# Performance work log

Hardware: AMD Instinct MI355X
Metric: run time of the kernel (lower is better)

Reference implementation:

```python
import jax, jax.numpy as jnp
import numpy as np

N = 100000   # num nodes
E = 500000   # num hyperedges
NNZ = 1600000
H, C = 4, 32
IN_CH = 128


def setup_inputs() -> dict:
    key = jax.random.key(0)
    k1, k2, k3, k4, k5 = jax.random.split(key, 5)
    X = jax.random.normal(k1, (N, IN_CH), dtype=jnp.float32)
    W = jax.random.normal(k2, (IN_CH, H * C), dtype=jnp.float32) * (1.0 / np.sqrt(IN_CH))
    att_e = jax.random.normal(k3, (1, H, C), dtype=jnp.float32) * 0.1
    vertex = jax.random.randint(k4, (NNZ,), 0, N, dtype=jnp.int64)
    edges = jax.random.randint(k5, (NNZ,), 0, E, dtype=jnp.int64)
    return {"X": X, "W": W, "att_e": att_e, "vertex": vertex, "edges": edges}


def reference(X, W, att_e, vertex, edges):
    n = X.shape[0]
    X0 = X @ W                                  # [N, H*C]
    Xh = X0.reshape(n, H, C)                    # [N, H, C]
    Xve = Xh[vertex]                            # [nnz, H, C] gather
    # scatter-mean over hyperedges
    esum = jax.ops.segment_sum(Xve, edges, num_segments=E)            # [E, H, C]
    cnt = jax.ops.segment_sum(jnp.ones((Xve.shape[0],), X.dtype), edges, num_segments=E)
    Xe = esum / jnp.maximum(cnt, 1.0)[:, None, None]                  # [E, H, C]
    # per-edge attention score
    alpha_e = (Xe * att_e).sum(-1)              # [E, H]
    a_ev = alpha_e[edges]                       # [nnz, H]
    alpha = jax.nn.leaky_relu(a_ev, 0.01)
    # segment softmax over vertex groups
    m = jax.ops.segment_max(alpha, vertex, num_segments=n)            # [N, H]
    ex = jnp.exp(alpha - m[vertex])
    den = jax.ops.segment_sum(ex, vertex, num_segments=n)             # [N, H]
    alpha = ex / (den[vertex] + 1e-16)          # [nnz, H]
    # weighted scatter-sum back to nodes
    Xev = Xe[edges] * alpha[:, :, None]         # [nnz, H, C]
    Xv = jax.ops.segment_sum(Xev, vertex, num_segments=n)             # [N, H, C]
    return Xv.reshape(n, H * C) + X0
```

## Files before the change

kernel.cpp:

```cpp
#include <hip/hip_runtime.h>
#include <hip/hip_bf16.h>
#include <hip/hip_fp16.h>
#include <cstdint>

#define NH 4
#define HC 128
#define INCH 128
#define NEDGE 500000
#define NN 100000

#define KE_SHIFT 11
#define KV_SHIFT 9
#define KE (1 << KE_SHIFT)
#define KV (1 << KV_SHIFT)
#define NBE 245
#define NBV 196
#define CAP_E 8192
#define CAP_V 10240
#define CHUNK_A 8192

typedef float          f32x2 __attribute__((ext_vector_type(2)));
typedef float          f32x4 __attribute__((ext_vector_type(4)));
typedef float          f32x8 __attribute__((ext_vector_type(8)));
typedef unsigned int   u32x2 __attribute__((ext_vector_type(2)));
typedef unsigned int   u32x4 __attribute__((ext_vector_type(4)));
typedef unsigned short u16x8 __attribute__((ext_vector_type(8)));

static __device__ __forceinline__ unsigned short f2bf(float f){
  union { float f; unsigned u; } v; v.f = f;
  unsigned r = v.u + 0x7fffu + ((v.u >> 16) & 1u);
  return (unsigned short)(r >> 16);
}
static __device__ __forceinline__ float bf2f(unsigned short b){
  union { unsigned u; float f; } v; v.u = ((unsigned)b) << 16;
  return v.f;
}
static __device__ __forceinline__ f32x8 bf8f(u16x8 b){
  f32x8 r;
  r[0]=bf2f(b[0]); r[1]=bf2f(b[1]); r[2]=bf2f(b[2]); r[3]=bf2f(b[3]);
  r[4]=bf2f(b[4]); r[5]=bf2f(b[5]); r[6]=bf2f(b[6]); r[7]=bf2f(b[7]);
  return r;
}

#if __has_builtin(__builtin_amdgcn_cvt_pk_fp8_f32) && __has_builtin(__builtin_amdgcn_cvt_pk_f32_fp8)
#define FP8_HW 1
#else
#define FP8_HW 0
#endif

#if !FP8_HW
static __device__ __forceinline__ unsigned enc1_fp8(float v){
  union{ __half h; unsigned short u; } c; c.h = __float2half(v);
  unsigned u = c.u;
  unsigned s = (u>>15)&1u, e=(u>>10)&31u, m=u&0x3FFu;
  int e8 = (int)e - 8;
  unsigned lsb = (m>>7)&1u;
  unsigned m8 = (m + 63u + lsb) >> 7;
  if (m8 == 8u){ m8 = 0u; e8 += 1; }
  if (e8 <= 0)  return s<<7;
  if (e8 >= 16) return (s<<7)|0x7Eu;
  return (s<<7)|((unsigned)e8<<3)|m8;
}
static __device__ __forceinline__ float dec1_fp8(unsigned b){
  unsigned s=(b>>7)&1u, e=(b>>3)&15u, m=b&7u;
  union{unsigned u; float f;} r;
  if (e==0u){ r.f = (float)m * 0.001953125f; if(s) r.f = -r.f; }
  else r.u = (s<<31)|((e+120u)<<23)|(m<<20);
  return r.f;
}
#endif

static __device__ __forceinline__ u32x2 pack8_fp8(const f32x8 v){
  u32x2 w;
#if FP8_HW
  int w0 = __builtin_amdgcn_cvt_pk_fp8_f32(v[0], v[1], 0, false);
  w0     = __builtin_amdgcn_cvt_pk_fp8_f32(v[2], v[3], w0, true);
  int w1 = __builtin_amdgcn_cvt_pk_fp8_f32(v[4], v[5], 0, false);
  w1     = __builtin_amdgcn_cvt_pk_fp8_f32(v[6], v[7], w1, true);
  w.x = (unsigned)w0; w.y = (unsigned)w1;
#else
  w.x = enc1_fp8(v[0]) | (enc1_fp8(v[1])<<8) | (enc1_fp8(v[2])<<16) | (enc1_fp8(v[3])<<24);
  w.y = enc1_fp8(v[4]) | (enc1_fp8(v[5])<<8) | (enc1_fp8(v[6])<<16) | (enc1_fp8(v[7])<<24);
#endif
  return w;
}
static __device__ __forceinline__ void fma8_fp8(f32x8& acc, float c, u32x2 q){
#if FP8_HW
  f32x2 p;
  p = __builtin_amdgcn_cvt_pk_f32_fp8((int)q.x, false); acc[0] += c*p.x; acc[1] += c*p.y;
  p = __builtin_amdgcn_cvt_pk_f32_fp8((int)q.x, true ); acc[2] += c*p.x; acc[3] += c*p.y;
  p = __builtin_amdgcn_cvt_pk_f32_fp8((int)q.y, false); acc[4] += c*p.x; acc[5] += c*p.y;
  p = __builtin_amdgcn_cvt_pk_f32_fp8((int)q.y, true ); acc[6] += c*p.x; acc[7] += c*p.y;
#else
  acc[0] += c*dec1_fp8(q.x&0xFF);        acc[1] += c*dec1_fp8((q.x>>8)&0xFF);
  acc[2] += c*dec1_fp8((q.x>>16)&0xFF);  acc[3] += c*dec1_fp8(q.x>>24);
  acc[4] += c*dec1_fp8(q.y&0xFF);        acc[5] += c*dec1_fp8((q.y>>8)&0xFF);
  acc[6] += c*dec1_fp8((q.y>>16)&0xFF);  acc[7] += c*dec1_fp8(q.y>>24);
#endif
}

#define GBM 128
#define GBK 16
__global__ __launch_bounds__(256) void gemm_x0(const float* __restrict__ X,
                                               const float* __restrict__ Wm,
                                               const float* __restrict__ att,
                                               unsigned short* __restrict__ X0bf,
                                               float* __restrict__ score, int nrows){
  __shared__ float As[GBK][GBM+4];
  __shared__ float Bs[GBK][HC+4];
  __shared__ float sc[GBM][17];
  const int tid  = threadIdx.x;
  const int row0 = blockIdx.x * GBM;
  const int trow = tid >> 4;
  const int tcol = tid & 15;
  float acc[8][8];
  #pragma unroll
  for (int i=0;i<8;i++)
    #pragma unroll
    for (int j=0;j<8;j++) acc[i][j]=0.f;

  for (int k0=0;k0<INCH;k0+=GBK){
    #pragma unroll
    for (int l = tid; l < 512; l += 256){
      int r  = l >> 2;
      int ks = (l & 3) * 4;
      int grow = row0 + r;
      float4 v = make_float4(0.f,0.f,0.f,0.f);
      if (grow < nrows) v = *(const float4*)(X + (size_t)grow*INCH + k0 + ks);
      As[ks+0][r]=v.x; As[ks+1][r]=v.y; As[ks+2][r]=v.z; As[ks+3][r]=v.w;
    }
    #pragma unroll
    for (int l = tid; l < 512; l += 256){
      int r  = l >> 5;
      int cs = (l & 31) * 4;
      float4 v = *(const float4*)(Wm + (size_t)(k0+r)*HC + cs);
      *(float4*)(&Bs[r][cs]) = v;
    }
    __syncthreads();
    #pragma unroll
    for (int kk=0;kk<GBK;kk++){
      float a[8], b[8];
      *(float4*)&a[0] = *(float4*)&As[kk][trow*8];
      *(float4*)&a[4] = *(float4*)&As[kk][trow*8+4];
      *(float4*)&b[0] = *(float4*)&Bs[kk][tcol*8];
      *(float4*)&b[4] = *(float4*)&Bs[kk][tcol*8+4];
      #pragma unroll
      for (int i=0;i<8;i++)
        #pragma unroll
        for (int j=0;j<8;j++) acc[i][j] = fmaf(a[i], b[j], acc[i][j]);
    }
    __syncthreads();
  }
  float attv[8];
  *(float4*)&attv[0] = *(const float4*)(att + tcol*8);
  *(float4*)&attv[4] = *(const float4*)(att + tcol*8 + 4);
  #pragma unroll
  for (int i=0;i<8;i++){
    int grow = row0 + trow*8 + i;
    float p = 0.f;
    #pragma unroll
    for (int j=0;j<8;j++) p = fmaf(acc[i][j], attv[j], p);
    sc[trow*8+i][tcol] = p;
    if (grow < nrows){
      ushort4 b0, b1;
      b0.x=f2bf(acc[i][0]); b0.y=f2bf(acc[i][1]); b0.z=f2bf(acc[i][2]); b0.w=f2bf(acc[i][3]);
      b1.x=f2bf(acc[i][4]); b1.y=f2bf(acc[i][5]); b1.z=f2bf(acc[i][6]); b1.w=f2bf(acc[i][7]);
      *(ushort4*)(X0bf + (size_t)grow*HC + tcol*8    ) = b0;
      *(ushort4*)(X0bf + (size_t)grow*HC + tcol*8 + 4) = b1;
    }
  }
  __syncthreads();
  for (int idx = tid; idx < GBM*NH; idx += 256){
    int row = idx >> 2, h = idx & 3;
    int grow = row0 + row;
    if (grow < nrows){
      float s = sc[row][4*h] + sc[row][4*h+1] + sc[row][4*h+2] + sc[row][4*h+3];
      score[(size_t)grow*NH + h] = s;
    }
  }
}

__global__ __launch_bounds__(512) void phaseA(const int* __restrict__ vertex,
                                              const int* __restrict__ edges, int nnz,
                                              int* __restrict__ cursE, int* __restrict__ cursV,
                                              unsigned* __restrict__ stgE, unsigned* __restrict__ stgV){
  __shared__ int cE[NBE], c2E[NBE], gE[NBE];
  __shared__ int cV[NBV], c2V[NBV], gV[NBV];
  const int t = threadIdx.x;
  const int base = blockIdx.x * CHUNK_A;
  int ev[16], vv[16];
  #pragma unroll
  for (int j=0;j<16;j++){
    int i = base + t + j*512;
    if (i < nnz){ ev[j] = edges[i]; vv[j] = vertex[i]; }
    else ev[j] = -1;
  }
  for (int j=t;j<NBE;j+=512){ cE[j]=0; c2E[j]=0; }
  for (int j=t;j<NBV;j+=512){ cV[j]=0; c2V[j]=0; }
  __syncthreads();
  #pragma unroll
  for (int j=0;j<16;j++) if (ev[j]>=0){
    atomicAdd(&cE[ev[j]>>KE_SHIFT], 1);
    atomicAdd(&cV[vv[j]>>KV_SHIFT], 1);
  }
  __syncthreads();
  for (int j=t;j<NBE;j+=512) gE[j] = atomicAdd(&cursE[j], cE[j]);
  for (int j=t;j<NBV;j+=512) gV[j] = atomicAdd(&cursV[j], cV[j]);
  __syncthreads();
  #pragma unroll
  for (int j=0;j<16;j++) if (ev[j]>=0){
    int bE = ev[j]>>KE_SHIFT;
    int p = gE[bE] + atomicAdd(&c2E[bE],1);
    if (p < CAP_E) stgE[(size_t)bE*CAP_E + p] = ((unsigned)vv[j] << KE_SHIFT) | (unsigned)(ev[j] & (KE-1));
    int bV = vv[j]>>KV_SHIFT;
    int q = gV[bV] + atomicAdd(&c2V[bV],1);
    if (q < CAP_V) stgV[(size_t)bV*CAP_V + q] = ((unsigned)ev[j] << KV_SHIFT) | (unsigned)(vv[j] & (KV-1));
  }
}

template<int K, int CAP, int IT, int SHIFT, int NB>
__global__ __launch_bounds__(512) void phaseB_k(const unsigned* __restrict__ stg,
                                                const int* __restrict__ curs,
                                                int* __restrict__ offsOut,
                                                int* __restrict__ csrOut, int nKeys){
  __shared__ int cur[K];
  __shared__ int tsum[512];
  __shared__ int bsh[512];
  const int b = blockIdx.x, t = threadIdx.x;
  const int k0 = b * K;
  const int kc = min(K, nKeys - k0);
  int c = (t < NB) ? min(curs[t], CAP) : 0;
  bsh[t] = c; __syncthreads();
  for (int d2=1; d2<512; d2<<=1){
    int x = (t>=d2) ? bsh[t-d2] : 0; __syncthreads();
    bsh[t] += x; __syncthreads();
  }
  const int gbase = (b > 0) ? bsh[b-1] : 0;
  const int cnt   = min(curs[b], CAP);
  if (b == NB-1 && t == 0) offsOut[nKeys] = bsh[NB-1];
  unsigned it[IT];
  #pragma unroll
  for (int j=0;j<IT;j++){
    int i = t + j*512;
    it[j] = (i < cnt) ? stg[(size_t)b*CAP + i] : 0xFFFFFFFFu;
  }
  for (int j=t;j<K;j+=512) cur[j] = 0;
  __syncthreads();
  #pragma unroll
  for (int j=0;j<IT;j++) if (it[j] != 0xFFFFFFFFu) atomicAdd(&cur[it[j] & (K-1)], 1);
  __syncthreads();
  constexpr int KPT = K / 512;
  int loc[KPT]; int s = 0;
  #pragma unroll
  for (int j=0;j<KPT;j++){ loc[j] = s; s += cur[t*KPT + j]; }
  tsum[t] = s; __syncthreads();
  for (int d2=1; d2<512; d2<<=1){
    int x = (t>=d2) ? tsum[t-d2] : 0; __syncthreads();
    tsum[t] += x; __syncthreads();
  }
  const int tbase = tsum[t] - s;
  __syncthreads();
  #pragma unroll
  for (int j=0;j<KPT;j++){
    int k = t*KPT + j;
    int abs0 = gbase + tbase + loc[j];
    if (k < kc) offsOut[k0 + k] = abs0;
    cur[k] = abs0;
  }
  __syncthreads();
  #pragma unroll
  for (int j=0;j<IT;j++) if (it[j] != 0xFFFFFFFFu){
    int pos = atomicAdd(&cur[it[j] & (K-1)], 1);
    csrOut[pos] = (int)(it[j] >> SHIFT);
  }
}

__global__ __launch_bounds__(256) void edge_agg(const unsigned short* __restrict__ X0bf,
                                                const float* __restrict__ score,
                                                const int* __restrict__ ecsr,
                                                const int* __restrict__ eoffs,
                                                unsigned char* __restrict__ Xe8,
                                                float* __restrict__ scaleE,
                                                float* __restrict__ alphaE, int E){
  int eg = blockIdx.x * 16 + (threadIdx.x >> 4);
  if (eg >= E) return;
  const int lane  = threadIdx.x & 15;
  const int cbase = lane * 8;
  const int start = eoffs[eg];
  const int d     = eoffs[eg+1] - start;
  f32x8 acc0 = {0.f,0.f,0.f,0.f,0.f,0.f,0.f,0.f};
  f32x8 acc1 = {0.f,0.f,0.f,0.f,0.f,0.f,0.f,0.f};
  float sacc0 = 0.f, sacc1 = 0.f;
  int k = 0;
  for (; k+1<d; k+=2){
    int v0 = ecsr[start + k];
    int v1 = ecsr[start + k + 1];
    u16x8 x0 = *(const u16x8*)(X0bf + (size_t)v0*HC + cbase);
    u16x8 x1 = *(const u16x8*)(X0bf + (size_t)v1*HC + cbase);
    if (lane < NH){
      sacc0 += score[(size_t)v0*NH + lane];
      sacc1 += score[(size_t)v1*NH + lane];
    }
    acc0 += bf8f(x0);
    acc1 += bf8f(x1);
  }
  if (k < d){
    int v0 = ecsr[start + k];
    u16x8 x0 = *(const u16x8*)(X0bf + (size_t)v0*HC + cbase);
    if (lane < NH) sacc0 += score[(size_t)v0*NH + lane];
    acc0 += bf8f(x0);
  }
  acc0 += acc1;
  const float inv = 1.0f / fmaxf((float)d, 1.0f);
  acc0 *= inv;
  float lm = fmaxf(fmaxf(fmaxf(fabsf(acc0[0]),fabsf(acc0[1])),fmaxf(fabsf(acc0[2]),fabsf(acc0[3]))),
                   fmaxf(fmaxf(fabsf(acc0[4]),fabsf(acc0[5])),fmaxf(fabsf(acc0[6]),fabsf(acc0[7]))));
  #pragma unroll
  for (int s=1; s<16; s<<=1) lm = fmaxf(lm, __shfl_xor(lm, s, 16));
  const float qs  = (lm > 1e-30f) ? 448.0f/lm : 0.f;
  const float dqs = (lm > 1e-30f) ? lm*(1.0f/448.0f) : 0.f;
  f32x8 q = acc0 * qs;
  u32x2 w = pack8_fp8(q);
  *(u32x2*)(Xe8 + (size_t)eg*HC + cbase) = w;
  if (lane == 4) scaleE[eg] = dqs;
  if (lane < NH){
    float a = (sacc0 + sacc1) * inv;
    a = a > 0.f ? a : 0.01f*a;
    alphaE[(size_t)eg*NH + lane] = a;
  }
}

__global__ __launch_bounds__(256) void vert_pass(const unsigned short* __restrict__ X0bf,
                                                 const unsigned char* __restrict__ Xe8,
                                                 const float* __restrict__ scaleE,
                                                 const float* __restrict__ alphaE,
                                                 const int* __restrict__ vcsr,
                                                 const int* __restrict__ voffs,
                                                 float* __restrict__ out, int N){
  int n = blockIdx.x * 16 + (threadIdx.x >> 4);
  if (n >= N) return;
  const int lane  = threadIdx.x & 15;
  const int cbase = lane * 8;
  const int h     = lane >> 2;
  const int j0    = lane & 3;
  const size_t obase = (size_t)n*HC + cbase;
  f32x8 x0 = bf8f(*(const u16x8*)(X0bf + obase));
  const int start = voffs[n];
  const int d     = voffs[n+1] - start;
  if (d == 0){
    f32x4 lo = {x0[0],x0[1],x0[2],x0[3]}, hi = {x0[4],x0[5],x0[6],x0[7]};
    __builtin_nontemporal_store(lo, (f32x4*)(out + obase));
    __builtin_nontemporal_store(hi, (f32x4*)(out + obase + 4));
    return;
  }

  float m = -1e30f, den = 0.f;
  for (int j=j0; j<d; j+=4){
    int e = vcsr[start + j];
    float a = alphaE[(size_t)e*NH + h];
    float mn = fmaxf(m, a);
    den = den*__expf(m - mn) + __expf(a - mn);
    m = mn;
  }
  #pragma unroll
  for (int s=1; s<4; s<<=1){
    float mo = __shfl_xor(m, s, 4);
    float dn = __shfl_xor(den, s, 4);
    float mn = fmaxf(m, mo);
    den = den*__expf(m - mn) + dn*__expf(mo - mn);
    m = mn;
  }
  const float w = 1.0f / (den + 1e-16f);

  f32x8 acc0 = {0.f,0.f,0.f,0.f,0.f,0.f,0.f,0.f};
  f32x8 acc1 = {0.f,0.f,0.f,0.f,0.f,0.f,0.f,0.f};
  f32x8 acc2 = {0.f,0.f,0.f,0.f,0.f,0.f,0.f,0.f};
  f32x8 acc3 = {0.f,0.f,0.f,0.f,0.f,0.f,0.f,0.f};
  int k = 0;
  for (; k+3<d; k+=4){
    int e0 = vcsr[start + k];
    int e1 = vcsr[start + k + 1];
    int e2 = vcsr[start + k + 2];
    int e3 = vcsr[start + k + 3];
    float a0 = alphaE[(size_t)e0*NH + h];
    float a1 = alphaE[(size_t)e1*NH + h];
    float a2 = alphaE[(size_t)e2*NH + h];
    float a3 = alphaE[(size_t)e3*NH + h];
    float r0 = scaleE[e0], r1 = scaleE[e1], r2 = scaleE[e2], r3 = scaleE[e3];
    u32x2 q0 = *(const u32x2*)(Xe8 + (size_t)e0*HC + cbase);
    u32x2 q1 = *(const u32x2*)(Xe8 + (size_t)e1*HC + cbase);
    u32x2 q2 = *(const u32x2*)(Xe8 + (size_t)e2*HC + cbase);
    u32x2 q3 = *(const u32x2*)(Xe8 + (size_t)e3*HC + cbase);
    fma8_fp8(acc0, __expf(a0 - m)*w*r0, q0);
    fma8_fp8(acc1, __expf(a1 - m)*w*r1, q1);
    fma8_fp8(acc2, __expf(a2 - m)*w*r2, q2);
    fma8_fp8(acc3, __expf(a3 - m)*w*r3, q3);
  }
  for (; k<d; k++){
    int e0 = vcsr[start + k];
    float a0 = alphaE[(size_t)e0*NH + h];
    float r0 = scaleE[e0];
    u32x2 q0 = *(const u32x2*)(Xe8 + (size_t)e0*HC + cbase);
    fma8_fp8(acc0, __expf(a0 - m)*w*r0, q0);
  }
  acc0 += acc1; acc2 += acc3; acc0 += acc2;
  acc0 += x0;
  f32x4 lo = {acc0[0],acc0[1],acc0[2],acc0[3]};
  f32x4 hi = {acc0[4],acc0[5],acc0[6],acc0[7]};
  __builtin_nontemporal_store(lo, (f32x4*)(out + obase));
  __builtin_nontemporal_store(hi, (f32x4*)(out + obase + 4));
}

extern "C" void kernel_launch(void* const* d_in, const int* in_sizes, int n_in,
                              void* d_out, int out_size, void* d_ws, size_t ws_size,
                              hipStream_t stream){
  const float* X   = (const float*)d_in[0];
  const float* Wm  = (const float*)d_in[1];
  const float* att = (const float*)d_in[2];
  const int* vertex = (const int*)d_in[3];
  const int* edges  = (const int*)d_in[4];
  const int N   = in_sizes[0] / INCH;
  const int NNZ = in_sizes[3];
  const int E   = NEDGE;

  char* ws = (char*)d_ws;
  size_t off = 0;
  auto alloc = [&](size_t bytes)->char*{
    char* p = ws + off;
    off += (bytes + 255) & ~(size_t)255;
    return p;
  };
  unsigned char*  Xe8    = (unsigned char*)alloc((size_t)E * HC);
  float*          scaleE = (float*)alloc((size_t)E * sizeof(float));
  unsigned short* X0bf   = (unsigned short*)alloc((size_t)NN * HC * sizeof(unsigned short));
  float*          score  = (float*)alloc((size_t)NN * NH * sizeof(float));
  float*          alphaE = (float*)alloc((size_t)E * NH * sizeof(float));
  int*            eoffs  = (int*)alloc((size_t)(E+1) * sizeof(int));
  int*            voffs  = (int*)alloc((size_t)(NN+1) * sizeof(int));
  int*            ecsr   = (int*)alloc((size_t)NNZ * sizeof(int));
  int*            vcsr   = (int*)alloc((size_t)NNZ * sizeof(int));
  int*            curs   = (int*)alloc((size_t)(NBE + NBV) * sizeof(int));
  int*            cursE  = curs;
  int*            cursV  = curs + NBE;
  unsigned* stgE = (unsigned*)(void*)Xe8;
  unsigned* stgV = (unsigned*)((char*)(void*)Xe8 + (size_t)NBE * CAP_E * sizeof(unsigned));

  gemm_x0<<<(N + GBM - 1)/GBM, 256, 0, stream>>>(X, Wm, att, X0bf, score, N);
  hipMemsetAsync(curs, 0, (size_t)(NBE + NBV) * sizeof(int), stream);
  phaseA<<<(NNZ + CHUNK_A - 1)/CHUNK_A, 512, 0, stream>>>(vertex, edges, NNZ, cursE, cursV, stgE, stgV);
  phaseB_k<KE, CAP_E, CAP_E/512, KE_SHIFT, NBE><<<NBE, 512, 0, stream>>>(stgE, cursE, eoffs, ecsr, E);
  phaseB_k<KV, CAP_V, CAP_V/512, KV_SHIFT, NBV><<<NBV, 512, 0, stream>>>(stgV, cursV, voffs, vcsr, NN);
  edge_agg<<<(E + 15)/16, 256, 0, stream>>>(X0bf, score, ecsr, eoffs, Xe8, scaleE, alphaE, E);
  vert_pass<<<(N + 15)/16, 256, 0, stream>>>(X0bf, Xe8, scaleE, alphaE, vcsr, voffs, (float*)d_out, N);
}
```

Before: 291.0 us.

## Fuse GEMM with bucketing, merge phaseB launches, single-pass online softmax in vert_pass

Runs the histogram/bucketing pass and the X@W GEMM in one launch by giving each block a role by index, and merges the two CSR-building phaseB launches into one grid. Edge alpha and fp8 dequant scale are interleaved into one record array so vert_pass needs one vector load per edge instead of two scattered loads. vert_pass switches from a two-pass softmax (max/denominator pass, then weighted sum) to a single-pass online softmax with four independent running max/accumulator sets merged at the end. This removes launch gaps and one full pass over the vertex adjacency, at the cost of extra exp and rescale work per edge and a halved bucketing chunk size.

```diff
diff --git a/kernel.cpp b/kernel.cpp
--- a/kernel.cpp
+++ b/kernel.cpp
@@ -17,13 +17,12 @@
 #define NBV 196
 #define CAP_E 8192
 #define CAP_V 10240
-#define CHUNK_A 8192
+#define CHUNK_A 4096
 
 typedef float          f32x2 __attribute__((ext_vector_type(2)));
 typedef float          f32x4 __attribute__((ext_vector_type(4)));
 typedef float          f32x8 __attribute__((ext_vector_type(8)));
 typedef unsigned int   u32x2 __attribute__((ext_vector_type(2)));
-typedef unsigned int   u32x4 __attribute__((ext_vector_type(4)));
 typedef unsigned short u16x8 __attribute__((ext_vector_type(8)));
 
 static __device__ __forceinline__ unsigned short f2bf(float f){
@@ -84,35 +83,76 @@
 #endif
   return w;
 }
-static __device__ __forceinline__ void fma8_fp8(f32x8& acc, float c, u32x2 q){
+static __device__ __forceinline__ void fma8s_fp8(f32x8& acc, float c, float w, u32x2 q){
 #if FP8_HW
   f32x2 p;
-  p = __builtin_amdgcn_cvt_pk_f32_fp8((int)q.x, false); acc[0] += c*p.x; acc[1] += c*p.y;
-  p = __builtin_amdgcn_cvt_pk_f32_fp8((int)q.x, true ); acc[2] += c*p.x; acc[3] += c*p.y;
-  p = __builtin_amdgcn_cvt_pk_f32_fp8((int)q.y, false); acc[4] += c*p.x; acc[5] += c*p.y;
-  p = __builtin_amdgcn_cvt_pk_f32_fp8((int)q.y, true ); acc[6] += c*p.x; acc[7] += c*p.y;
+  p = __builtin_amdgcn_cvt_pk_f32_fp8((int)q.x, false); acc[0]=acc[0]*c + w*p.x; acc[1]=acc[1]*c + w*p.y;
+  p = __builtin_amdgcn_cvt_pk_f32_fp8((int)q.x, true ); acc[2]=acc[2]*c + w*p.x; acc[3]=acc[3]*c + w*p.y;
+  p = __builtin_amdgcn_cvt_pk_f32_fp8((int)q.y, false); acc[4]=acc[4]*c + w*p.x; acc[5]=acc[5]*c + w*p.y;
+  p = __builtin_amdgcn_cvt_pk_f32_fp8((int)q.y, true ); acc[6]=acc[6]*c + w*p.x; acc[7]=acc[7]*c + w*p.y;
 #else
-  acc[0] += c*dec1_fp8(q.x&0xFF);        acc[1] += c*dec1_fp8((q.x>>8)&0xFF);
-  acc[2] += c*dec1_fp8((q.x>>16)&0xFF);  acc[3] += c*dec1_fp8(q.x>>24);
-  acc[4] += c*dec1_fp8(q.y&0xFF);        acc[5] += c*dec1_fp8((q.y>>8)&0xFF);
-  acc[6] += c*dec1_fp8((q.y>>16)&0xFF);  acc[7] += c*dec1_fp8(q.y>>24);
+  acc[0]=acc[0]*c + w*dec1_fp8(q.x&0xFF);        acc[1]=acc[1]*c + w*dec1_fp8((q.x>>8)&0xFF);
+  acc[2]=acc[2]*c + w*dec1_fp8((q.x>>16)&0xFF);  acc[3]=acc[3]*c + w*dec1_fp8(q.x>>24);
+  acc[4]=acc[4]*c + w*dec1_fp8(q.y&0xFF);        acc[5]=acc[5]*c + w*dec1_fp8((q.y>>8)&0xFF);
+  acc[6]=acc[6]*c + w*dec1_fp8((q.y>>16)&0xFF);  acc[7]=acc[7]*c + w*dec1_fp8(q.y>>24);
 #endif
 }
 
 #define GBM 128
 #define GBK 16
-__global__ __launch_bounds__(256) void gemm_x0(const float* __restrict__ X,
-                                               const float* __restrict__ Wm,
-                                               const float* __restrict__ att,
-                                               unsigned short* __restrict__ X0bf,
-                                               float* __restrict__ score, int nrows){
+__global__ __launch_bounds__(256) void gemmA_fused(const float* __restrict__ X,
+                                                   const float* __restrict__ Wm,
+                                                   const float* __restrict__ att,
+                                                   unsigned short* __restrict__ X0bf,
+                                                   float* __restrict__ score, int nrows,
+                                                   const int* __restrict__ vertex,
+                                                   const int* __restrict__ edges, int nnz,
+                                                   int* __restrict__ cursE, int* __restrict__ cursV,
+                                                   unsigned* __restrict__ stgE, unsigned* __restrict__ stgV,
+                                                   int nA){
   __shared__ float As[GBK][GBM+4];
   __shared__ float Bs[GBK][HC+4];
   __shared__ float sc[GBM][17];
-  const int tid  = threadIdx.x;
-  const int row0 = blockIdx.x * GBM;
-  const int trow = tid >> 4;
-  const int tcol = tid & 15;
+  __shared__ int cE[NBE], c2E[NBE], gE[NBE];
+  __shared__ int cV[NBV], c2V[NBV], gV[NBV];
+  const int t = threadIdx.x;
+
+  if ((int)blockIdx.x < nA){
+    const int base = blockIdx.x * CHUNK_A;
+    int ev[16], vv[16];
+    #pragma unroll
+    for (int j=0;j<16;j++){
+      int i = base + t + j*256;
+      if (i < nnz){ ev[j] = edges[i]; vv[j] = vertex[i]; }
+      else ev[j] = -1;
+    }
+    for (int j=t;j<NBE;j+=256){ cE[j]=0; c2E[j]=0; }
+    for (int j=t;j<NBV;j+=256){ cV[j]=0; c2V[j]=0; }
+    __syncthreads();
+    #pragma unroll
+    for (int j=0;j<16;j++) if (ev[j]>=0){
+      atomicAdd(&cE[ev[j]>>KE_SHIFT], 1);
+      atomicAdd(&cV[vv[j]>>KV_SHIFT], 1);
+    }
+    __syncthreads();
+    for (int j=t;j<NBE;j+=256) gE[j] = atomicAdd(&cursE[j], cE[j]);
+    for (int j=t;j<NBV;j+=256) gV[j] = atomicAdd(&cursV[j], cV[j]);
+    __syncthreads();
+    #pragma unroll
+    for (int j=0;j<16;j++) if (ev[j]>=0){
+      int bE = ev[j]>>KE_SHIFT;
+      int p = gE[bE] + atomicAdd(&c2E[bE],1);
+      if (p < CAP_E) stgE[(size_t)bE*CAP_E + p] = ((unsigned)vv[j] << KE_SHIFT) | (unsigned)(ev[j] & (KE-1));
+      int bV = vv[j]>>KV_SHIFT;
+      int q = gV[bV] + atomicAdd(&c2V[bV],1);
+      if (q < CAP_V) stgV[(size_t)bV*CAP_V + q] = ((unsigned)ev[j] << KV_SHIFT) | (unsigned)(vv[j] & (KV-1));
+    }
+    return;
+  }
+
+  const int row0 = (blockIdx.x - nA) * GBM;
+  const int trow = t >> 4;
+  const int tcol = t & 15;
   float acc[8][8];
   #pragma unroll
   for (int i=0;i<8;i++)
@@ -121,7 +161,7 @@
 
   for (int k0=0;k0<INCH;k0+=GBK){
     #pragma unroll
-    for (int l = tid; l < 512; l += 256){
+    for (int l = t; l < 512; l += 256){
       int r  = l >> 2;
       int ks = (l & 3) * 4;
       int grow = row0 + r;
@@ -130,7 +170,7 @@
       As[ks+0][r]=v.x; As[ks+1][r]=v.y; As[ks+2][r]=v.z; As[ks+3][r]=v.w;
     }
     #pragma unroll
-    for (int l = tid; l < 512; l += 256){
+    for (int l = t; l < 512; l += 256){
       int r  = l >> 5;
       int cs = (l & 31) * 4;
       float4 v = *(const float4*)(Wm + (size_t)(k0+r)*HC + cs);
@@ -170,7 +210,7 @@
     }
   }
   __syncthreads();
-  for (int idx = tid; idx < GBM*NH; idx += 256){
+  for (int idx = t; idx < GBM*NH; idx += 256){
     int row = idx >> 2, h = idx & 3;
     int grow = row0 + row;
     if (grow < nrows){
@@ -180,53 +220,13 @@
   }
 }
 
-__global__ __launch_bounds__(512) void phaseA(const int* __restrict__ vertex,
-                                              const int* __restrict__ edges, int nnz,
-                                              int* __restrict__ cursE, int* __restrict__ cursV,
-                                              unsigned* __restrict__ stgE, unsigned* __restrict__ stgV){
-  __shared__ int cE[NBE], c2E[NBE], gE[NBE];
-  __shared__ int cV[NBV], c2V[NBV], gV[NBV];
+template<int K, int CAP, int IT, int SHIFT, int NB>
+__device__ __forceinline__ void phaseB_body(const unsigned* __restrict__ stg,
+                                            const int* __restrict__ curs,
+                                            int* __restrict__ offsOut,
+                                            int* __restrict__ csrOut, int nKeys, int b,
+                                            int* cur, int* tsum, int* bsh){
   const int t = threadIdx.x;
-  const int base = blockIdx.x * CHUNK_A;
-  int ev[16], vv[16];
-  #pragma unroll
-  for (int j=0;j<16;j++){
-    int i = base + t + j*512;
-    if (i < nnz){ ev[j] = edges[i]; vv[j] = vertex[i]; }
-    else ev[j] = -1;
-  }
-  for (int j=t;j<NBE;j+=512){ cE[j]=0; c2E[j]=0; }
-  for (int j=t;j<NBV;j+=512){ cV[j]=0; c2V[j]=0; }
-  __syncthreads();
-  #pragma unroll
-  for (int j=0;j<16;j++) if (ev[j]>=0){
-    atomicAdd(&cE[ev[j]>>KE_SHIFT], 1);
-    atomicAdd(&cV[vv[j]>>KV_SHIFT], 1);
-  }
-  __syncthreads();
-  for (int j=t;j<NBE;j+=512) gE[j] = atomicAdd(&cursE[j], cE[j]);
-  for (int j=t;j<NBV;j+=512) gV[j] = atomicAdd(&cursV[j], cV[j]);
-  __syncthreads();
-  #pragma unroll
-  for (int j=0;j<16;j++) if (ev[j]>=0){
-    int bE = ev[j]>>KE_SHIFT;
-    int p = gE[bE] + atomicAdd(&c2E[bE],1);
-    if (p < CAP_E) stgE[(size_t)bE*CAP_E + p] = ((unsigned)vv[j] << KE_SHIFT) | (unsigned)(ev[j] & (KE-1));
-    int bV = vv[j]>>KV_SHIFT;
-    int q = gV[bV] + atomicAdd(&c2V[bV],1);
-    if (q < CAP_V) stgV[(size_t)bV*CAP_V + q] = ((unsigned)ev[j] << KV_SHIFT) | (unsigned)(vv[j] & (KV-1));
-  }
-}
-
-template<int K, int CAP, int IT, int SHIFT, int NB>
-__global__ __launch_bounds__(512) void phaseB_k(const unsigned* __restrict__ stg,
-                                                const int* __restrict__ curs,
-                                                int* __restrict__ offsOut,
-                                                int* __restrict__ csrOut, int nKeys){
-  __shared__ int cur[K];
-  __shared__ int tsum[512];
-  __shared__ int bsh[512];
-  const int b = blockIdx.x, t = threadIdx.x;
   const int k0 = b * K;
   const int kc = min(K, nKeys - k0);
   int c = (t < NB) ? min(curs[t], CAP) : 0;
@@ -275,13 +275,26 @@
   }
 }
 
+__global__ __launch_bounds__(512) void phaseB_fused(const unsigned* __restrict__ stgE,
+                                                    const unsigned* __restrict__ stgV,
+                                                    const int* __restrict__ cursE,
+                                                    const int* __restrict__ cursV,
+                                                    int* __restrict__ eoffs, int* __restrict__ voffs,
+                                                    int* __restrict__ ecsr, int* __restrict__ vcsr){
+  __shared__ int cur[KE];
+  __shared__ int tsum[512];
+  __shared__ int bsh[512];
+  const int b = blockIdx.x;
+  if (b < NBE) phaseB_body<KE, CAP_E, CAP_E/512, KE_SHIFT, NBE>(stgE, cursE, eoffs, ecsr, NEDGE, b, cur, tsum, bsh);
+  else         phaseB_body<KV, CAP_V, CAP_V/512, KV_SHIFT, NBV>(stgV, cursV, voffs, vcsr, NN, b - NBE, cur, tsum, bsh);
+}
+
 __global__ __launch_bounds__(256) void edge_agg(const unsigned short* __restrict__ X0bf,
                                                 const float* __restrict__ score,
                                                 const int* __restrict__ ecsr,
                                                 const int* __restrict__ eoffs,
                                                 unsigned char* __restrict__ Xe8,
-                                                float* __restrict__ scaleE,
-                                                float* __restrict__ alphaE, int E){
+                                                float* __restrict__ alphaS, int E){
   int eg = blockIdx.x * 16 + (threadIdx.x >> 4);
   if (eg >= E) return;
   const int lane  = threadIdx.x & 15;
@@ -322,18 +335,17 @@
   f32x8 q = acc0 * qs;
   u32x2 w = pack8_fp8(q);
   *(u32x2*)(Xe8 + (size_t)eg*HC + cbase) = w;
-  if (lane == 4) scaleE[eg] = dqs;
   if (lane < NH){
     float a = (sacc0 + sacc1) * inv;
     a = a > 0.f ? a : 0.01f*a;
-    alphaE[(size_t)eg*NH + lane] = a;
+    f32x2 rec = { a, dqs };
+    *(f32x2*)(alphaS + (size_t)eg*8 + lane*2) = rec;
   }
 }
 
 __global__ __launch_bounds__(256) void vert_pass(const unsigned short* __restrict__ X0bf,
                                                  const unsigned char* __restrict__ Xe8,
-                                                 const float* __restrict__ scaleE,
-                                                 const float* __restrict__ alphaE,
+                                                 const float* __restrict__ alphaS,
                                                  const int* __restrict__ vcsr,
                                                  const int* __restrict__ voffs,
                                                  float* __restrict__ out, int N){
@@ -341,8 +353,7 @@
   if (n >= N) return;
   const int lane  = threadIdx.x & 15;
   const int cbase = lane * 8;
-  const int h     = lane >> 2;
-  const int j0    = lane & 3;
+  const int h2    = (lane >> 2) * 2;
   const size_t obase = (size_t)n*HC + cbase;
   f32x8 x0 = bf8f(*(const u16x8*)(X0bf + obase));
   const int start = voffs[n];
@@ -354,59 +365,56 @@
     return;
   }
 
-  float m = -1e30f, den = 0.f;
-  for (int j=j0; j<d; j+=4){
-    int e = vcsr[start + j];
-    float a = alphaE[(size_t)e*NH + h];
-    float mn = fmaxf(m, a);
-    den = den*__expf(m - mn) + __expf(a - mn);
-    m = mn;
-  }
-  #pragma unroll
-  for (int s=1; s<4; s<<=1){
-    float mo = __shfl_xor(m, s, 4);
-    float dn = __shfl_xor(den, s, 4);
-    float mn = fmaxf(m, mo);
-    den = den*__expf(m - mn) + dn*__expf(mo - mn);
-    m = mn;
-  }
-  const float w = 1.0f / (den + 1e-16f);
-
+  float m0=-1e30f, m1=-1e30f, m2=-1e30f, m3=-1e30f;
+  float den0=0.f, den1=0.f, den2=0.f, den3=0.f;
   f32x8 acc0 = {0.f,0.f,0.f,0.f,0.f,0.f,0.f,0.f};
   f32x8 acc1 = {0.f,0.f,0.f,0.f,0.f,0.f,0.f,0.f};
   f32x8 acc2 = {0.f,0.f,0.f,0.f,0.f,0.f,0.f,0.f};
   f32x8 acc3 = {0.f,0.f,0.f,0.f,0.f,0.f,0.f,0.f};
+
+#define UPD(i, ar, q) { \
+    float mn_ = fmaxf(m##i, (ar).x); \
+    float c_  = __expf(m##i - mn_); \
+    float p_  = __expf((ar).x - mn_); \
+    den##i = den##i * c_ + p_; \
+    fma8s_fp8(acc##i, c_, p_ * (ar).y, (q)); \
+    m##i = mn_; }
+
   int k = 0;
   for (; k+3<d; k+=4){
     int e0 = vcsr[start + k];
     int e1 = vcsr[start + k + 1];
     int e2 = vcsr[start + k + 2];
     int e3 = vcsr[start + k + 3];
-    float a0 = alphaE[(size_t)e0*NH + h];
-    float a1 = alphaE[(size_t)e1*NH + h];
-    float a2 = alphaE[(size_t)e2*NH + h];
-    float a3 = alphaE[(size_t)e3*NH + h];
-    float r0 = scaleE[e0], r1 = scaleE[e1], r2 = scaleE[e2], r3 = scaleE[e3];
+    f32x2 ar0 = *(const f32x2*)(alphaS + (size_t)e0*8 + h2);
+    f32x2 ar1 = *(const f32x2*)(alphaS + (size_t)e1*8 + h2);
+    f32x2 ar2 = *(const f32x2*)(alphaS + (size_t)e2*8 + h2);
+    f32x2 ar3 = *(const f32x2*)(alphaS + (size_t)e3*8 + h2);
     u32x2 q0 = *(const u32x2*)(Xe8 + (size_t)e0*HC + cbase);
     u32x2 q1 = *(const u32x2*)(Xe8 + (size_t)e1*HC + cbase);
     u32x2 q2 = *(const u32x2*)(Xe8 + (size_t)e2*HC + cbase);
     u32x2 q3 = *(const u32x2*)(Xe8 + (size_t)e3*HC + cbase);
-    fma8_fp8(acc0, __expf(a0 - m)*w*r0, q0);
-    fma8_fp8(acc1, __expf(a1 - m)*w*r1, q1);
-    fma8_fp8(acc2, __expf(a2 - m)*w*r2, q2);
-    fma8_fp8(acc3, __expf(a3 - m)*w*r3, q3);
+    UPD(0, ar0, q0);
+    UPD(1, ar1, q1);
+    UPD(2, ar2, q2);
+    UPD(3, ar3, q3);
   }
   for (; k<d; k++){
     int e0 = vcsr[start + k];
-    float a0 = alphaE[(size_t)e0*NH + h];
-    float r0 = scaleE[e0];
+    f32x2 ar0 = *(const f32x2*)(alphaS + (size_t)e0*8 + h2);
     u32x2 q0 = *(const u32x2*)(Xe8 + (size_t)e0*HC + cbase);
-    fma8_fp8(acc0, __expf(a0 - m)*w*r0, q0);
-  }
-  acc0 += acc1; acc2 += acc3; acc0 += acc2;
-  acc0 += x0;
-  f32x4 lo = {acc0[0],acc0[1],acc0[2],acc0[3]};
-  f32x4 hi = {acc0[4],acc0[5],acc0[6],acc0[7]};
+    UPD(0, ar0, q0);
+  }
+#undef UPD
+
+  float mn = fmaxf(fmaxf(m0,m1), fmaxf(m2,m3));
+  float c0 = __expf(m0-mn), c1 = __expf(m1-mn), c2 = __expf(m2-mn), c3 = __expf(m3-mn);
+  float den = den0*c0 + den1*c1 + den2*c2 + den3*c3;
+  f32x8 acc = acc0*c0 + acc1*c1 + acc2*c2 + acc3*c3;
+  const float w = 1.0f / (den + 1e-16f);
+  acc = acc*w + x0;
+  f32x4 lo = {acc[0],acc[1],acc[2],acc[3]};
+  f32x4 hi = {acc[4],acc[5],acc[6],acc[7]};
   __builtin_nontemporal_store(lo, (f32x4*)(out + obase));
   __builtin_nontemporal_store(hi, (f32x4*)(out + obase + 4));
 }
@@ -431,10 +439,9 @@
     return p;
   };
   unsigned char*  Xe8    = (unsigned char*)alloc((size_t)E * HC);
-  float*          scaleE = (float*)alloc((size_t)E * sizeof(float));
   unsigned short* X0bf   = (unsigned short*)alloc((size_t)NN * HC * sizeof(unsigned short));
   float*          score  = (float*)alloc((size_t)NN * NH * sizeof(float));
-  float*          alphaE = (float*)alloc((size_t)E * NH * sizeof(float));
+  float*          alphaS = (float*)alloc((size_t)E * 8 * sizeof(float));
   int*            eoffs  = (int*)alloc((size_t)(E+1) * sizeof(int));
   int*            voffs  = (int*)alloc((size_t)(NN+1) * sizeof(int));
   int*            ecsr   = (int*)alloc((size_t)NNZ * sizeof(int));
@@ -445,11 +452,13 @@
   unsigned* stgE = (unsigned*)(void*)Xe8;
   unsigned* stgV = (unsigned*)((char*)(void*)Xe8 + (size_t)NBE * CAP_E * sizeof(unsigned));
 
-  gemm_x0<<<(N + GBM - 1)/GBM, 256, 0, stream>>>(X, Wm, att, X0bf, score, N);
+  const int nGemm = (N + GBM - 1) / GBM;
+  const int nA    = (NNZ + CHUNK_A - 1) / CHUNK_A;
+
   hipMemsetAsync(curs, 0, (size_t)(NBE + NBV) * sizeof(int), stream);
-  phaseA<<<(NNZ + CHUNK_A - 1)/CHUNK_A, 512, 0, stream>>>(vertex, edges, NNZ, cursE, cursV, stgE, stgV);
-  phaseB_k<KE, CAP_E, CAP_E/512, KE_SHIFT, NBE><<<NBE, 512, 0, stream>>>(stgE, cursE, eoffs, ecsr, E);
-  phaseB_k<KV, CAP_V, CAP_V/512, KV_SHIFT, NBV><<<NBV, 512, 0, stream>>>(stgV, cursV, voffs, vcsr, NN);
-  edge_agg<<<(E + 15)/16, 256, 0, stream>>>(X0bf, score, ecsr, eoffs, Xe8, scaleE, alphaE, E);
-  vert_pass<<<(N + 15)/16, 256, 0, stream>>>(X0bf, Xe8, scaleE, alphaE, vcsr, voffs, (float*)d_out, N);
-}
+  gemmA_fused<<<nA + nGemm, 256, 0, stream>>>(X, Wm, att, X0bf, score, N,
+                                              vertex, edges, NNZ, cursE, cursV, stgE, stgV, nA);
+  phaseB_fused<<<NBE + NBV, 512, 0, stream>>>(stgE, stgV, cursE, cursV, eoffs, voffs, ecsr, vcsr);
+  edge_agg<<<(E + 15)/16, 256, 0, stream>>>(X0bf, score, ecsr, eoffs, Xe8, alphaS, E);
+  vert_pass<<<(N + 15)/16, 256, 0, stream>>>(X0bf, Xe8, alphaS, vcsr, voffs, (float*)d_out, N);
+}
```

After: 256.8 us. 11.7% less time.
